# Optimization experiments

Hardware: AMD Instinct MI355X
Metric: run time of the kernel (lower is better)

Reference implementation:

```python
import jax, jax.numpy as jnp
import numpy as np

D_MODEL = 1024
N_HEADS = 16
HEAD_DIM = D_MODEL // N_HEADS  # d_keys = d_values = 64
EPS = 1e-10


def setup_inputs() -> dict:
    key = jax.random.key(0)
    ks = jax.random.split(key, 11)
    N, L, S = 4, 4096, 4096
    inp = {
        'queries': jax.random.normal(ks[0], (N, L, D_MODEL), jnp.float32),
        'keys': jax.random.normal(ks[1], (N, S, D_MODEL), jnp.float32),
        'values': jax.random.normal(ks[2], (N, S, D_MODEL), jnp.float32),
        # Dense layer params (glorot-ish scale)
        'Wq': jax.random.normal(ks[3], (D_MODEL, D_MODEL), jnp.float32) / np.sqrt(D_MODEL),
        'bq': jnp.zeros((D_MODEL,), jnp.float32),
        'Wk': jax.random.normal(ks[4], (D_MODEL, D_MODEL), jnp.float32) / np.sqrt(D_MODEL),
        'bk': jnp.zeros((D_MODEL,), jnp.float32),
        'Wv': jax.random.normal(ks[5], (D_MODEL, D_MODEL), jnp.float32) / np.sqrt(D_MODEL),
        'bv': jnp.zeros((D_MODEL,), jnp.float32),
        'Wo': jax.random.normal(ks[6], (D_MODEL, D_MODEL), jnp.float32) / np.sqrt(D_MODEL),
        'bo': jnp.zeros((D_MODEL,), jnp.float32),
    }
    return inp


def _feat(x):
    # elu(x) + 1 feature map (strictly positive)
    return jax.nn.elu(x) + 1.0


def reference(queries, keys, values, Wq, bq, Wk, bk, Wv, bv, Wo, bo):
    N, L, _ = queries.shape
    S = keys.shape[1]
    H, Dh = N_HEADS, HEAD_DIM
    # projections -> [n, l, h, d]
    Q = (queries @ Wq + bq).reshape(N, L, H, Dh)
    K = (keys @ Wk + bk).reshape(N, S, H, Dh)
    V = (values @ Wv + bv).reshape(N, S, H, Dh)
    Q_lin = _feat(Q)
    K_lin = _feat(K)
    # normalizer Z: [n, l, h]
    K_sum = K_lin.sum(axis=1)  # [n, h, d]
    Z = 1.0 / (jnp.einsum('nlhd,nhd->nlh', Q_lin, K_sum) + EPS)
    # KV outer-product accumulation: [n, h, m, d]
    KV = jnp.einsum('nshd,nshm->nhmd', K_lin, V)
    # attention output: [n, l, h, m]
    V_lin = jnp.einsum('nlhd,nhmd,nlh->nlhm', Q_lin, KV, Z)
    new_values = V_lin.reshape(N, L, H * Dh)
    return new_values @ Wo + bo
```

## Files before the change

kernel.cpp:

```cpp
#include <hip/hip_runtime.h>
#include <hip/hip_bf16.h>
#include <stdint.h>

#define D_MODEL 1024
#define NHEADS  16
#define DH      64
#define NBATCH  4
#define SEQLEN  4096
#define MROWS   (NBATCH*SEQLEN)
#define EPSV    1e-10f

typedef __hip_bfloat16 bf16;
typedef unsigned short ushort_t;
typedef __attribute__((ext_vector_type(8))) short short8;
typedef __attribute__((ext_vector_type(4))) float f32x4;

struct __align__(8) bf16x4s { bf16 a, b, c, d; };

__device__ __forceinline__ void async_copy16(void* lds, const void* g) {
  __builtin_amdgcn_global_load_lds(
      (const __attribute__((address_space(1))) unsigned int*)(uintptr_t)g,
      (__attribute__((address_space(3))) unsigned int*)(uintptr_t)lds,
      16, 0, 0);
}

__global__ __launch_bounds__(256)
void cvt_bf16(const float* __restrict__ s, bf16* __restrict__ d) {
  const int i = blockIdx.x * 256 + threadIdx.x;
  const f32x4 v = ((const f32x4*)s)[i];
  bf16x4s o;
  o.a = __float2bfloat16(v[0]);
  o.b = __float2bfloat16(v[1]);
  o.c = __float2bfloat16(v[2]);
  o.d = __float2bfloat16(v[3]);
  ((bf16x4s*)d)[i] = o;
}

__global__ void transpose4(const float* __restrict__ s0, const float* __restrict__ s1,
                           const float* __restrict__ s2, const float* __restrict__ s3,
                           bf16* __restrict__ d0, bf16* __restrict__ d1,
                           bf16* __restrict__ d2, bf16* __restrict__ d3) {
  const float* s; bf16* d;
  switch (blockIdx.z) {
    case 0: s = s0; d = d0; break;
    case 1: s = s1; d = d1; break;
    case 2: s = s2; d = d2; break;
    default: s = s3; d = d3; break;
  }
  __shared__ float tile[32][33];
  int x = blockIdx.x*32 + threadIdx.x;
  int y = blockIdx.y*32 + threadIdx.y;
  tile[threadIdx.y][threadIdx.x] = s[(size_t)y*D_MODEL + x];
  __syncthreads();
  int xo = blockIdx.y*32 + threadIdx.x;
  int yo = blockIdx.x*32 + threadIdx.y;
  d[(size_t)yo*D_MODEL + xo] = __float2bfloat16(tile[threadIdx.x][threadIdx.y]);
}

__device__ __forceinline__ void storeC(float* p, float v) { *p = v; }
__device__ __forceinline__ void storeC(bf16*  p, float v) { *p = __float2bfloat16(v); }

template<int ACT, int TRANS, typename CT>
__global__ __launch_bounds__(512, 4)
void gemm_bias_act(const bf16* __restrict__ A, const bf16* __restrict__ BT,
                   const float* __restrict__ bias, CT* __restrict__ C,
                   int M, int N, int K) {
  __shared__ __align__(16) short Asm[2][128*32];
  __shared__ __align__(16) short Bsm[2][256*32];
  const int tid  = threadIdx.x;
  const int wave = tid >> 6;
  const int lane = tid & 63;

  const int nbx = N >> 8;
  const int nwg = (M >> 7) * nbx;
  int fid = blockIdx.y * nbx + blockIdx.x;
  fid = (fid & 7) * (nwg >> 3) + (fid >> 3);
  const int m0 = (fid / nbx) * 128;
  const int n0 = (fid % nbx) * 256;

  const int wr = wave >> 2, wc = wave & 3;
  const int srow = tid >> 2;
  const int ldst = (tid & 3) * 8;
  const int sgrp = ((tid & 3) ^ ((srow >> 1) & 3)) * 8;
  const int fr   = lane & 15;
  const int quad = lane >> 4;
  const int sslot = (quad ^ ((fr >> 1) & 3)) * 8;

  f32x4 acc[4][4] = {};
  const int nk = K / 32;

  async_copy16(&Asm[0][srow*32 + ldst], A + (size_t)(m0+srow)*K + sgrp);
  #pragma unroll
  for (int r = 0; r < 2; ++r) {
    const int row = r*128 + srow;
    async_copy16(&Bsm[0][row*32 + ldst], BT + (size_t)(n0+row)*K + sgrp);
  }

  int cur = 0;
  for (int t = 0; t < nk; ++t) {
    if (t + 1 < nk) {
      const int k0n = (t + 1) * 32;
      async_copy16(&Asm[cur^1][srow*32 + ldst], A + (size_t)(m0+srow)*K + k0n + sgrp);
      #pragma unroll
      for (int r = 0; r < 2; ++r) {
        const int row = r*128 + srow;
        async_copy16(&Bsm[cur^1][row*32 + ldst], BT + (size_t)(n0+row)*K + k0n + sgrp);
      }
      asm volatile("s_waitcnt vmcnt(3)" ::: "memory");
    } else {
      asm volatile("s_waitcnt vmcnt(0)" ::: "memory");
    }
    asm volatile("s_barrier" ::: "memory");

    short8 afr[4], bfr[4];
    #pragma unroll
    for (int i = 0; i < 4; ++i)
      afr[i] = *(const short8*)&Asm[cur][(wr*64 + i*16 + fr)*32 + sslot];
    #pragma unroll
    for (int j = 0; j < 4; ++j)
      bfr[j] = *(const short8*)&Bsm[cur][(wc*64 + j*16 + fr)*32 + sslot];

    __builtin_amdgcn_s_setprio(1);
    #pragma unroll
    for (int i = 0; i < 4; ++i)
      #pragma unroll
      for (int j = 0; j < 4; ++j)
        acc[i][j] = __builtin_amdgcn_mfma_f32_16x16x32_bf16(afr[i], bfr[j], acc[i][j], 0, 0, 0);
    __builtin_amdgcn_s_setprio(0);

    asm volatile("s_barrier" ::: "memory");
    cur ^= 1;
  }

  #pragma unroll
  for (int j = 0; j < 4; ++j) {
    const int gn = n0 + wc*64 + j*16 + fr;
    const float bv = bias[gn];
    #pragma unroll
    for (int i = 0; i < 4; ++i) {
      const int gm = m0 + wr*64 + i*16 + quad*4;
      if (TRANS) {
        float vv[4];
        #pragma unroll
        for (int r2 = 0; r2 < 4; ++r2) {
          float v = acc[i][j][r2] + bv;
          if (ACT) v = (v > 0.f) ? (v + 1.f) : __expf(v);
          vv[r2] = v;
        }
        bf16x4s o{__float2bfloat16(vv[0]), __float2bfloat16(vv[1]),
                  __float2bfloat16(vv[2]), __float2bfloat16(vv[3])};
        *(bf16x4s*)((bf16*)C + (size_t)gn*M + gm) = o;
      } else {
        #pragma unroll
        for (int r2 = 0; r2 < 4; ++r2) {
          float v = acc[i][j][r2] + bv;
          if (ACT) v = (v > 0.f) ? (v + 1.f) : __expf(v);
          storeC(&C[(size_t)(gm + r2)*N + gn], v);
        }
      }
    }
  }
}

#define KV_SPLIT 16
__global__ __launch_bounds__(256)
void kv_kernel(const bf16* __restrict__ KT, const bf16* __restrict__ VT,
               float* __restrict__ KVp, float* __restrict__ Ksp) {
  const int b  = blockIdx.x;
  const int sp = b & (KV_SPLIT-1);
  const int nh = b >> 4;
  const int h = nh & (NHEADS-1), n = nh >> 4;
  const int tid = threadIdx.x;
  const int w = tid >> 6, lane = tid & 63;
  const int fr = lane & 15, quad = lane >> 4;

  __shared__ __align__(16) short Kt[64*256];
  __shared__ __align__(16) short Vt[64*256];

  const size_t cbase = (size_t)n*SEQLEN + sp*(SEQLEN/KV_SPLIT);
  const bf16* KTh = KT + (size_t)(h*DH)*MROWS + cbase;
  const bf16* VTh = VT + (size_t)(h*DH)*MROWS + cbase;

  const int lr = lane >> 5;
  const int g  = lane & 31;
  #pragma unroll
  for (int i = 0; i < 8; ++i) {
    const int row = (i*4 + w)*2 + lr;
    const int sg = g ^ (row & 7);
    async_copy16(&Kt[row*256 + g*8], KTh + (size_t)row*MROWS + sg*8);
  }
  #pragma unroll
  for (int i = 0; i < 8; ++i) {
    const int row = (i*4 + w)*2 + lr;
    const int sg = g ^ (row & 7);
    async_copy16(&Vt[row*256 + g*8], VTh + (size_t)row*MROWS + sg*8);
  }
  __syncthreads();

  f32x4 acc[4] = {};
  f32x4 ksacc[4] = {};
  const short8 ones8 = {0x3F80,0x3F80,0x3F80,0x3F80,0x3F80,0x3F80,0x3F80,0x3F80};
  const int arow = w*16 + fr;

  #pragma unroll
  for (int ks = 0; ks < 8; ++ks) {
    const int gq = ks*4 + quad;
    const short8 av = *(const short8*)&Vt[arow*256 + ((gq ^ (arow & 7)) << 3)];
    #pragma unroll
    for (int j = 0; j < 4; ++j) {
      const int brow = j*16 + fr;
      const short8 bk = *(const short8*)&Kt[brow*256 + ((gq ^ (brow & 7)) << 3)];
      acc[j] = __builtin_amdgcn_mfma_f32_16x16x32_bf16(av, bk, acc[j], 0, 0, 0);
      if (w == 0)
        ksacc[j] = __builtin_amdgcn_mfma_f32_16x16x32_bf16(ones8, bk, ksacc[j], 0, 0, 0);
    }
  }

  float* outp = KVp + (size_t)b*4096;
  #pragma unroll
  for (int j = 0; j < 4; ++j)
    #pragma unroll
    for (int r = 0; r < 4; ++r)
      outp[(w*16 + quad*4 + r)*64 + j*16 + fr] = acc[j][r];

  if (tid < 16)
    #pragma unroll
    for (int j = 0; j < 4; ++j)
      Ksp[b*64 + j*16 + tid] = ksacc[j][0];
}

__global__ __launch_bounds__(256)
void kv_reduce(const float* __restrict__ KVp, const float* __restrict__ Ksp,
               bf16* __restrict__ KVb) {
  const int c  = blockIdx.x;
  const int nh = blockIdx.y;
  const int tid = threadIdx.x;
  const int e = c*1024 + tid*4;
  const int m = e >> 6, d = e & 63;
  f32x4 s = {};
  #pragma unroll
  for (int sp = 0; sp < KV_SPLIT; ++sp)
    s += *(const f32x4*)(KVp + ((size_t)(nh*KV_SPLIT + sp))*4096 + e);

  bf16* base = KVb + (size_t)nh*(144*64);
  bf16 h0 = __float2bfloat16(s[0]), h1 = __float2bfloat16(s[1]);
  bf16 h2 = __float2bfloat16(s[2]), h3 = __float2bfloat16(s[3]);
  bf16x4s hi4{h0, h1, h2, h3};
  bf16x4s lo4{__float2bfloat16(s[0] - __bfloat162float(h0)),
              __float2bfloat16(s[1] - __bfloat162float(h1)),
              __float2bfloat16(s[2] - __bfloat162float(h2)),
              __float2bfloat16(s[3] - __bfloat162float(h3))};
  *(bf16x4s*)&base[m*64 + d]        = hi4;
  *(bf16x4s*)&base[(64 + m)*64 + d] = lo4;

  if (c == 0) {
    if (tid < 64) {
      float ks = 0.f;
      #pragma unroll
      for (int sp = 0; sp < KV_SPLIT; ++sp)
        ks += Ksp[(nh*KV_SPLIT + sp)*64 + tid];
      bf16 hh = __float2bfloat16(ks);
      base[128*64 + tid] = hh;
      base[129*64 + tid] = __float2bfloat16(ks - __bfloat162float(hh));
    }
    for (int i2 = tid; i2 < 14*64; i2 += 256)
      base[130*64 + i2] = __float2bfloat16(0.0f);
  }
}

__global__ __launch_bounds__(256)
void vlin_kernel(const bf16* __restrict__ Ql, const bf16* __restrict__ KVb,
                 bf16* __restrict__ Vl) {
  const int lc = blockIdx.x;
  const int nh = blockIdx.y;
  const int h = nh & (NHEADS-1), n = nh >> 4;
  const int tid = threadIdx.x, wave = tid >> 6, lane = tid & 63;
  const int fr = lane & 15, quad = lane >> 4;

  __shared__ __align__(16) short Qs[128*64];

  const int l0 = lc * 128;
  const size_t qbase = ((size_t)(n*SEQLEN) + l0)*D_MODEL + h*DH;
  const int lr8 = lane >> 3;
  const int g8  = lane & 7;
  #pragma unroll
  for (int i = 0; i < 4; ++i) {
    const int row = (i*4 + wave)*8 + lr8;
    const int sg = g8 ^ (row & 7);
    async_copy16(&Qs[row*64 + g8*8], Ql + qbase + (size_t)row*D_MODEL + sg*8);
  }
  __syncthreads();

  short8 afr[2][2];
  #pragma unroll
  for (int i = 0; i < 2; ++i)
    #pragma unroll
    for (int ks = 0; ks < 2; ++ks) {
      const int arow = wave*32 + i*16 + fr;
      afr[i][ks] = *(const short8*)&Qs[arow*64 + (((ks*4 + quad) ^ (fr & 7)) << 3)];
    }

  const bf16* bb = KVb + (size_t)nh*(144*64);
  f32x4 acc[2][9] = {};
  #pragma unroll
  for (int ks = 0; ks < 2; ++ks) {
    #pragma unroll
    for (int j = 0; j < 9; ++j) {
      const short8 bfr = *(const short8*)(bb + (j*16 + fr)*64 + ks*32 + quad*8);
      #pragma unroll
      for (int i = 0; i < 2; ++i)
        acc[i][j] = __builtin_amdgcn_mfma_f32_16x16x32_bf16(afr[i][ks], bfr, acc[i][j], 0, 0, 0);
    }
  }

  #pragma unroll
  for (int i = 0; i < 2; ++i) {
    #pragma unroll
    for (int r2 = 0; r2 < 4; ++r2) {
      const float v = acc[i][8][r2];
      const float vp = v + __shfl_xor(v, 1, 64);
      const float z = 1.0f / (__shfl(vp, lane & 48, 64) + EPSV);
      const int rloc = wave*32 + i*16 + quad*4 + r2;
      #pragma unroll
      for (int j = 0; j < 4; ++j) {
        const float num = acc[i][j][r2] + acc[i][4 + j][r2];
        Vl[qbase + (size_t)rloc*D_MODEL + j*16 + fr] = __float2bfloat16(num * z);
      }
    }
  }
}

extern "C" void kernel_launch(void* const* d_in, const int* in_sizes, int n_in,
                              void* d_out, int out_size, void* d_ws, size_t ws_size,
                              hipStream_t stream) {
  const float* q  = (const float*)d_in[0];
  const float* k  = (const float*)d_in[1];
  const float* v  = (const float*)d_in[2];
  const float* Wq = (const float*)d_in[3];
  const float* bq = (const float*)d_in[4];
  const float* Wk = (const float*)d_in[5];
  const float* bk = (const float*)d_in[6];
  const float* Wv = (const float*)d_in[7];
  const float* bv = (const float*)d_in[8];
  const float* Wo = (const float*)d_in[9];
  const float* bo = (const float*)d_in[10];
  float* out = (float*)d_out;

  bf16* WqT = (bf16*)d_ws;
  bf16* WkT = WqT + (size_t)D_MODEL*D_MODEL;
  bf16* WvT = WkT + (size_t)D_MODEL*D_MODEL;
  bf16* WoT = WvT + (size_t)D_MODEL*D_MODEL;
  bf16* Xb  = WoT + (size_t)D_MODEL*D_MODEL;
  bf16* Ql  = Xb  + (size_t)MROWS*D_MODEL;
  bf16* Kl  = Ql  + (size_t)MROWS*D_MODEL;
  bf16* Vb  = Kl  + (size_t)MROWS*D_MODEL;
  bf16* Vl  = Kl;
  bf16* KVb = Vb + (size_t)MROWS*D_MODEL;
  float* KVp = (float*)Xb;
  float* Ksp = KVp + (size_t)NBATCH*NHEADS*KV_SPLIT*DH*DH;

  transpose4<<<dim3(32,32,4), dim3(32,32,1), 0, stream>>>(Wq,Wk,Wv,Wo, WqT,WkT,WvT,WoT);

  const int nconv4 = MROWS*D_MODEL/4;
  dim3 gb(512), gg(D_MODEL/256, MROWS/128);

  cvt_bf16<<<nconv4/256, 256, 0, stream>>>(q, Xb);
  gemm_bias_act<1,0,bf16><<<gg, gb, 0, stream>>>(Xb, WqT, bq, Ql, MROWS, D_MODEL, D_MODEL);
  cvt_bf16<<<nconv4/256, 256, 0, stream>>>(k, Xb);
  gemm_bias_act<1,1,bf16><<<gg, gb, 0, stream>>>(Xb, WkT, bk, Kl, MROWS, D_MODEL, D_MODEL);
  cvt_bf16<<<nconv4/256, 256, 0, stream>>>(v, Xb);
  gemm_bias_act<0,1,bf16><<<gg, gb, 0, stream>>>(Xb, WvT, bv, Vb, MROWS, D_MODEL, D_MODEL);

  kv_kernel<<<dim3(NBATCH*NHEADS*KV_SPLIT), dim3(256), 0, stream>>>(Kl, Vb, KVp, Ksp);
  kv_reduce<<<dim3(4, NBATCH*NHEADS), dim3(256), 0, stream>>>(KVp, Ksp, KVb);
  vlin_kernel<<<dim3(SEQLEN/128, NBATCH*NHEADS), dim3(256), 0, stream>>>(Ql, KVb, Vl);

  gemm_bias_act<0,0,float><<<gg, gb, 0, stream>>>(Vl, WoT, bo, out, MROWS, D_MODEL, D_MODEL);
}
```

Measured before the change: 463.4 us.

## Fuse fp32-to-bf16 input conversion into projection GEMM A-tile loading

Removes the three separate cvt_bf16 passes over queries/keys/values. The projection GEMMs now load fp32 A rows into registers, convert them to bf16 and write them into LDS, while B still uses async copies. A prefetch is restructured two steps ahead with register double buffering. This saves the write and re-read of a bf16 copy of each input, but the GEMM now reads fp32 A (twice the bytes per tile, repeated across the 4 column blocks) and gains extra barriers and register pressure.

```diff
diff --git a/kernel.cpp b/kernel.cpp
--- a/kernel.cpp
+++ b/kernel.cpp
@@ -24,16 +24,19 @@
       16, 0, 0);
 }
 
-__global__ __launch_bounds__(256)
-void cvt_bf16(const float* __restrict__ s, bf16* __restrict__ d) {
-  const int i = blockIdx.x * 256 + threadIdx.x;
-  const f32x4 v = ((const f32x4*)s)[i];
-  bf16x4s o;
-  o.a = __float2bfloat16(v[0]);
-  o.b = __float2bfloat16(v[1]);
-  o.c = __float2bfloat16(v[2]);
-  o.d = __float2bfloat16(v[3]);
-  ((bf16x4s*)d)[i] = o;
+__device__ __forceinline__ short8 cvt8(const f32x4& a, const f32x4& b) {
+  short8 w;
+  #pragma unroll
+  for (int e = 0; e < 4; ++e) {
+    bf16 x = __float2bfloat16(a[e]);
+    short s; __builtin_memcpy(&s, &x, 2); w[e] = s;
+  }
+  #pragma unroll
+  for (int e = 0; e < 4; ++e) {
+    bf16 x = __float2bfloat16(b[e]);
+    short s; __builtin_memcpy(&s, &x, 2); w[4 + e] = s;
+  }
+  return w;
 }
 
 __global__ void transpose4(const float* __restrict__ s0, const float* __restrict__ s1,
@@ -60,9 +63,9 @@
 __device__ __forceinline__ void storeC(float* p, float v) { *p = v; }
 __device__ __forceinline__ void storeC(bf16*  p, float v) { *p = __float2bfloat16(v); }
 
-template<int ACT, int TRANS, typename CT>
+template<int ACT, int TRANS, int AF32, typename AT, typename CT>
 __global__ __launch_bounds__(512, 4)
-void gemm_bias_act(const bf16* __restrict__ A, const bf16* __restrict__ BT,
+void gemm_bias_act(const AT* __restrict__ A, const bf16* __restrict__ BT,
                    const float* __restrict__ bias, CT* __restrict__ C,
                    int M, int N, int K) {
   __shared__ __align__(16) short Asm[2][128*32];
@@ -89,47 +92,108 @@
   f32x4 acc[4][4] = {};
   const int nk = K / 32;
 
-  async_copy16(&Asm[0][srow*32 + ldst], A + (size_t)(m0+srow)*K + sgrp);
-  #pragma unroll
-  for (int r = 0; r < 2; ++r) {
-    const int row = r*128 + srow;
-    async_copy16(&Bsm[0][row*32 + ldst], BT + (size_t)(n0+row)*K + sgrp);
-  }
-
-  int cur = 0;
-  for (int t = 0; t < nk; ++t) {
-    if (t + 1 < nk) {
-      const int k0n = (t + 1) * 32;
-      async_copy16(&Asm[cur^1][srow*32 + ldst], A + (size_t)(m0+srow)*K + k0n + sgrp);
-      #pragma unroll
-      for (int r = 0; r < 2; ++r) {
-        const int row = r*128 + srow;
-        async_copy16(&Bsm[cur^1][row*32 + ldst], BT + (size_t)(n0+row)*K + k0n + sgrp);
+#define FRAG_MFMA(c_) {                                                      \
+    short8 afr[4], bfr[4];                                                   \
+    _Pragma("unroll") for (int i = 0; i < 4; ++i)                            \
+      afr[i] = *(const short8*)&Asm[c_][(wr*64 + i*16 + fr)*32 + sslot];     \
+    _Pragma("unroll") for (int j = 0; j < 4; ++j)                            \
+      bfr[j] = *(const short8*)&Bsm[c_][(wc*64 + j*16 + fr)*32 + sslot];     \
+    __builtin_amdgcn_s_setprio(1);                                           \
+    _Pragma("unroll") for (int i = 0; i < 4; ++i)                            \
+    _Pragma("unroll") for (int j = 0; j < 4; ++j)                            \
+      acc[i][j] = __builtin_amdgcn_mfma_f32_16x16x32_bf16(afr[i], bfr[j],    \
+                                                          acc[i][j], 0,0,0);\
+    __builtin_amdgcn_s_setprio(0);                                           \
+  }
+
+  if constexpr (!AF32) {
+    const bf16* Ab = (const bf16*)A;
+    async_copy16(&Asm[0][srow*32 + ldst], Ab + (size_t)(m0+srow)*K + sgrp);
+    #pragma unroll
+    for (int r = 0; r < 2; ++r) {
+      const int row = r*128 + srow;
+      async_copy16(&Bsm[0][row*32 + ldst], BT + (size_t)(n0+row)*K + sgrp);
+    }
+    int cur = 0;
+    for (int t = 0; t < nk; ++t) {
+      if (t + 1 < nk) {
+        const int k0n = (t + 1) * 32;
+        async_copy16(&Asm[cur^1][srow*32 + ldst], Ab + (size_t)(m0+srow)*K + k0n + sgrp);
+        #pragma unroll
+        for (int r = 0; r < 2; ++r) {
+          const int row = r*128 + srow;
+          async_copy16(&Bsm[cur^1][row*32 + ldst], BT + (size_t)(n0+row)*K + k0n + sgrp);
+        }
+        asm volatile("s_waitcnt vmcnt(3)" ::: "memory");
+      } else {
+        asm volatile("s_waitcnt vmcnt(0)" ::: "memory");
       }
-      asm volatile("s_waitcnt vmcnt(3)" ::: "memory");
-    } else {
-      asm volatile("s_waitcnt vmcnt(0)" ::: "memory");
-    }
-    asm volatile("s_barrier" ::: "memory");
-
-    short8 afr[4], bfr[4];
-    #pragma unroll
-    for (int i = 0; i < 4; ++i)
-      afr[i] = *(const short8*)&Asm[cur][(wr*64 + i*16 + fr)*32 + sslot];
-    #pragma unroll
-    for (int j = 0; j < 4; ++j)
-      bfr[j] = *(const short8*)&Bsm[cur][(wc*64 + j*16 + fr)*32 + sslot];
-
-    __builtin_amdgcn_s_setprio(1);
-    #pragma unroll
-    for (int i = 0; i < 4; ++i)
-      #pragma unroll
-      for (int j = 0; j < 4; ++j)
-        acc[i][j] = __builtin_amdgcn_mfma_f32_16x16x32_bf16(afr[i], bfr[j], acc[i][j], 0, 0, 0);
-    __builtin_amdgcn_s_setprio(0);
-
-    asm volatile("s_barrier" ::: "memory");
-    cur ^= 1;
+      asm volatile("s_barrier" ::: "memory");
+      FRAG_MFMA(cur)
+      asm volatile("s_barrier" ::: "memory");
+      cur ^= 1;
+    }
+  } else {
+    const float* Af = (const float*)A;
+    const int ag = tid & 3;
+    const int apslot = (ag ^ ((srow >> 1) & 3)) * 8;
+    const float* Arow = Af + (size_t)(m0 + srow)*K + ag*8;
+
+#define ALOAD(ra, rb, kt) { const float* p_ = Arow + (size_t)(kt)*32;        \
+      ra = *(const f32x4*)p_;  rb = *(const f32x4*)(p_ + 4); }
+#define AWRITE(ra, rb, d_) { *(short8*)&Asm[d_][srow*32 + apslot] = cvt8(ra, rb); }
+#define STAGEB(d_, kt) { _Pragma("unroll") for (int r_ = 0; r_ < 2; ++r_) {  \
+      const int row_ = r_*128 + srow;                                        \
+      async_copy16(&Bsm[d_][row_*32 + ldst],                                 \
+                   BT + (size_t)(n0+row_)*K + (size_t)(kt)*32 + sgrp); } }
+
+    f32x4 s0a, s0b, s1a, s1b;
+
+    ALOAD(s0a, s0b, 0);
+    STAGEB(0, 0);
+    ALOAD(s1a, s1b, 1);
+    STAGEB(1, 1);
+    asm volatile("s_waitcnt vmcnt(4)" ::: "memory");
+    AWRITE(s0a, s0b, 0);
+    asm volatile("s_waitcnt lgkmcnt(0)" ::: "memory");
+
+#define GBODY(t, LA, LB, WA, WB) {                                           \
+    const int c_ = (t) & 1;                                                  \
+    asm volatile("s_barrier" ::: "memory");                  \
+    short8 afr[4], bfr[4];                                                   \
+    _Pragma("unroll") for (int i = 0; i < 4; ++i)                            \
+      afr[i] = *(const short8*)&Asm[c_][(wr*64 + i*16 + fr)*32 + sslot];     \
+    _Pragma("unroll") for (int j = 0; j < 4; ++j)                            \
+      bfr[j] = *(const short8*)&Bsm[c_][(wc*64 + j*16 + fr)*32 + sslot];     \
+    asm volatile("s_waitcnt lgkmcnt(0)" ::: "memory");    \
+    asm volatile("s_barrier" ::: "memory");                  \
+    if ((t) + 2 < nk) {                                                      \
+      ALOAD(LA, LB, (t) + 2);                                                \
+      STAGEB(c_, (t) + 2);                                                   \
+      asm volatile("s_waitcnt vmcnt(4)" ::: "memory");                       \
+    } else {                                                                 \
+      asm volatile("s_waitcnt vmcnt(0)" ::: "memory");                       \
+    }                                                                        \
+    if ((t) + 1 < nk) {                                                      \
+      AWRITE(WA, WB, c_ ^ 1);                                                \
+      asm volatile("s_waitcnt lgkmcnt(0)" ::: "memory");                     \
+    }                                                                        \
+    __builtin_amdgcn_s_setprio(1);                                           \
+    _Pragma("unroll") for (int i = 0; i < 4; ++i)                            \
+    _Pragma("unroll") for (int j = 0; j < 4; ++j)                            \
+      acc[i][j] = __builtin_amdgcn_mfma_f32_16x16x32_bf16(afr[i], bfr[j],    \
+                                                          acc[i][j], 0,0,0);\
+    __builtin_amdgcn_s_setprio(0);                                           \
+  }
+
+    for (int t = 0; t < nk; t += 2) {
+      GBODY(t,     s0a, s0b, s1a, s1b)
+      GBODY(t + 1, s1a, s1b, s0a, s0b)
+    }
+#undef GBODY
+#undef ALOAD
+#undef AWRITE
+#undef STAGEB
   }
 
   #pragma unroll
@@ -160,6 +224,7 @@
       }
     }
   }
+#undef FRAG_MFMA
 }
 
 #define KV_SPLIT 16
@@ -350,30 +415,25 @@
   bf16* WkT = WqT + (size_t)D_MODEL*D_MODEL;
   bf16* WvT = WkT + (size_t)D_MODEL*D_MODEL;
   bf16* WoT = WvT + (size_t)D_MODEL*D_MODEL;
-  bf16* Xb  = WoT + (size_t)D_MODEL*D_MODEL;
-  bf16* Ql  = Xb  + (size_t)MROWS*D_MODEL;
+  bf16* Ql  = WoT + (size_t)D_MODEL*D_MODEL;
   bf16* Kl  = Ql  + (size_t)MROWS*D_MODEL;
   bf16* Vb  = Kl  + (size_t)MROWS*D_MODEL;
   bf16* Vl  = Kl;
   bf16* KVb = Vb + (size_t)MROWS*D_MODEL;
-  float* KVp = (float*)Xb;
+  float* KVp = (float*)(KVb + (size_t)64*144*64);
   float* Ksp = KVp + (size_t)NBATCH*NHEADS*KV_SPLIT*DH*DH;
 
   transpose4<<<dim3(32,32,4), dim3(32,32,1), 0, stream>>>(Wq,Wk,Wv,Wo, WqT,WkT,WvT,WoT);
 
-  const int nconv4 = MROWS*D_MODEL/4;
   dim3 gb(512), gg(D_MODEL/256, MROWS/128);
 
-  cvt_bf16<<<nconv4/256, 256, 0, stream>>>(q, Xb);
-  gemm_bias_act<1,0,bf16><<<gg, gb, 0, stream>>>(Xb, WqT, bq, Ql, MROWS, D_MODEL, D_MODEL);
-  cvt_bf16<<<nconv4/256, 256, 0, stream>>>(k, Xb);
-  gemm_bias_act<1,1,bf16><<<gg, gb, 0, stream>>>(Xb, WkT, bk, Kl, MROWS, D_MODEL, D_MODEL);
-  cvt_bf16<<<nconv4/256, 256, 0, stream>>>(v, Xb);
-  gemm_bias_act<0,1,bf16><<<gg, gb, 0, stream>>>(Xb, WvT, bv, Vb, MROWS, D_MODEL, D_MODEL);
+  gemm_bias_act<1,0,1,float,bf16><<<gg, gb, 0, stream>>>(q, WqT, bq, Ql, MROWS, D_MODEL, D_MODEL);
+  gemm_bias_act<1,1,1,float,bf16><<<gg, gb, 0, stream>>>(k, WkT, bk, Kl, MROWS, D_MODEL, D_MODEL);
+  gemm_bias_act<0,1,1,float,bf16><<<gg, gb, 0, stream>>>(v, WvT, bv, Vb, MROWS, D_MODEL, D_MODEL);
 
   kv_kernel<<<dim3(NBATCH*NHEADS*KV_SPLIT), dim3(256), 0, stream>>>(Kl, Vb, KVp, Ksp);
   kv_reduce<<<dim3(4, NBATCH*NHEADS), dim3(256), 0, stream>>>(KVp, Ksp, KVb);
   vlin_kernel<<<dim3(SEQLEN/128, NBATCH*NHEADS), dim3(256), 0, stream>>>(Ql, KVb, Vl);
 
-  gemm_bias_act<0,0,float><<<gg, gb, 0, stream>>>(Vl, WoT, bo, out, MROWS, D_MODEL, D_MODEL);
-}
+  gemm_bias_act<0,0,0,bf16,float><<<gg, gb, 0, stream>>>(Vl, WoT, bo, out, MROWS, D_MODEL, D_MODEL);
+}
```

Result: slower. 510.5 us (+10.2%).
